# Optimization experiments

Hardware: AMD Instinct MI355X
Metric: run time of the kernel (lower is better)

The kernel has to match this reference:

```python
import jax, jax.numpy as jnp
import numpy as np

H = 1024  # hidden size
T = 4096  # sequence length


def setup_inputs() -> dict:
    key = jax.random.key(0)
    ks = jax.random.split(key, 11)
    s = 1.0 / np.sqrt(H)  # torch LSTM/Linear default init scale
    u = lambda k, shape: jax.random.uniform(k, shape, jnp.float32, -s, s)
    return {
        "x": jax.random.normal(ks[0], (1, T, 2), jnp.float32),
        # layer 0 (input size 2)
        "W_ih0": u(ks[1], (4 * H, 2)),
        "W_hh0": u(ks[2], (4 * H, H)),
        "b_ih0": u(ks[3], (4 * H,)),
        "b_hh0": u(ks[4], (4 * H,)),
        # layers 1-2 (input size H), stacked
        "W_ih12": u(ks[5], (2, 4 * H, H)),
        "W_hh12": u(ks[6], (2, 4 * H, H)),
        "b_ih12": u(ks[7], (2, 4 * H)),
        "b_hh12": u(ks[8], (2, 4 * H)),
        # output head Linear(H, 1)
        "W_res": u(ks[9], (1, H)),
        "b_res": u(ks[10], (1,)),
    }


def reference(x, W_ih0, W_hh0, b_ih0, b_hh0, W_ih12, W_hh12, b_ih12, b_hh12, W_res, b_res):
    xs = x[0]  # (T, 2); BATCH == 1
    W_ihs = [W_ih0, W_ih12[0], W_ih12[1]]
    W_hhs = [W_hh0, W_hh12[0], W_hh12[1]]
    b_ihs = [b_ih0, b_ih12[0], b_ih12[1]]
    b_hhs = [b_hh0, b_hh12[0], b_hh12[1]]

    def cell(inp, h, c, W_ih, W_hh, b_ih, b_hh):
        # PyTorch gate order: input, forget, cell(g), output
        gates = W_ih @ inp + b_ih + W_hh @ h + b_hh  # (4H,)
        i, f, g, o = jnp.split(gates, 4)
        i = jax.nn.sigmoid(i)
        f = jax.nn.sigmoid(f)
        g = jnp.tanh(g)
        o = jax.nn.sigmoid(o)
        c_new = f * c + i * g
        h_new = o * jnp.tanh(c_new)
        return h_new, c_new

    def step(carry, x_t):
        h, c = carry  # each (3, H)
        inp = x_t
        hs, cs = [], []
        for l in range(3):  # fixed small layer loop
            h_new, c_new = cell(inp, h[l], c[l], W_ihs[l], W_hhs[l], b_ihs[l], b_hhs[l])
            hs.append(h_new)
            cs.append(c_new)
            inp = h_new
        return (jnp.stack(hs), jnp.stack(cs)), inp  # emit top-layer h

    h0 = jnp.zeros((3, H), x.dtype)
    c0 = jnp.zeros((3, H), x.dtype)
    _, ys = jax.lax.scan(step, (h0, c0), xs)  # ys: (T, H)
    y = jax.nn.sigmoid(ys @ W_res.T + b_res)  # (T, 1)
    return y.reshape(1, T)
```

## Files before the change

kernel.cpp:

```cpp
#include <hip/hip_runtime.h>

#define HSZ 1024
#define TSTEPS 4096
#define NBLK 256
#define NTHR 256
#define HV (HSZ / 4)
#define REP_BYTES 24576

typedef _Float16 half2v __attribute__((ext_vector_type(2)));

#if __has_builtin(__builtin_amdgcn_fdot2)
#define FDOT2(a, b, c) __builtin_amdgcn_fdot2((a), (b), (c), false)
#else
__device__ __forceinline__ float FDOT2(half2v a, half2v b, float c) {
    return c + (float)a.x * (float)b.x + (float)a.y * (float)b.y;
}
#endif

__device__ __forceinline__ int f2i(float f) { int i; __builtin_memcpy(&i, &f, 4); return i; }
__device__ __forceinline__ float i2f(int i) { float f; __builtin_memcpy(&f, &i, 4); return f; }

template <int CTRL, int RM>
__device__ __forceinline__ float dpp_acc(float v) {
    int t = __builtin_amdgcn_update_dpp(0, f2i(v), CTRL, RM, 0xf, true);
    return v + i2f(t);
}
__device__ __forceinline__ float wave_sum63(float v) {
    v = dpp_acc<0x111, 0xf>(v);
    v = dpp_acc<0x112, 0xf>(v);
    v = dpp_acc<0x114, 0xf>(v);
    v = dpp_acc<0x118, 0xf>(v);
    v = dpp_acc<0x142, 0xa>(v);
    v = dpp_acc<0x143, 0xc>(v);
    return v;
}

__device__ __forceinline__ float sigm(float x) { return 1.0f / (1.0f + __expf(-x)); }
__device__ __forceinline__ float tanh_fast(float x) {
    const float e = __expf(2.0f * x);
    return 1.0f - 2.0f / (e + 1.0f);
}

__device__ __forceinline__ unsigned long long ld_coh64(const unsigned long long* p) {
    return __hip_atomic_load(p, __ATOMIC_RELAXED, __HIP_MEMORY_SCOPE_AGENT);
}
__device__ __forceinline__ void st_coh32(unsigned* p, unsigned v) {
    __hip_atomic_store(p, v, __ATOMIC_RELAXED, __HIP_MEMORY_SCOPE_AGENT);
}

__device__ __forceinline__ unsigned f16bits(float v) {
    _Float16 h = (_Float16)v;
    unsigned short b;
    __builtin_memcpy(&b, &h, 2);
    return (unsigned)b;
}

#define PINH(h) asm volatile("" : "+v"(h))

__device__ __forceinline__ half2v cvt2(float a, float b) {
    half2v r; r.x = (_Float16)a; r.y = (_Float16)b; return r;
}

__device__ __forceinline__ half2v bits_to_h2(unsigned v) {
    half2v h; __builtin_memcpy(&h, &v, 4); return h;
}

__device__ __forceinline__ unsigned pack_payload(unsigned long long q) {
#if __has_builtin(__builtin_amdgcn_perm)
    return __builtin_amdgcn_perm((unsigned)(q >> 32), (unsigned)q, 0x05040100u);
#else
    return ((unsigned)q & 0xFFFFu) | ((unsigned)(q >> 32) << 16);
#endif
}

struct PollA { unsigned long long q[8]; };

__device__ __forceinline__ PollA poll_issueA(const unsigned long long* A, int lane) {
    PollA p;
#pragma unroll
    for (int i = 0; i < 4; ++i) {
        p.q[2 * i]     = ld_coh64(A + 2 * lane + 128 * i);
        p.q[2 * i + 1] = ld_coh64(A + 2 * lane + 128 * i + 1);
    }
    return p;
}

__device__ __forceinline__ void poll_completeA(PollA& p, const unsigned long long* A,
                                               unsigned e, int lane, half2v* hf) {
    const unsigned long long K =
        ((unsigned long long)e << 16) | ((unsigned long long)e << 48);
    unsigned long long bad = 0;
#pragma unroll
    for (int j = 0; j < 8; ++j) bad |= (p.q[j] ^ K);
    bad &= 0xFFFF0000FFFF0000ull;
    while (!__all(bad == 0)) {
        __builtin_amdgcn_s_sleep(1);
        if (bad) {
#pragma unroll
            for (int i = 0; i < 4; ++i) {
                p.q[2 * i]     = ld_coh64(A + 2 * lane + 128 * i);
                p.q[2 * i + 1] = ld_coh64(A + 2 * lane + 128 * i + 1);
            }
            bad = 0;
#pragma unroll
            for (int j = 0; j < 8; ++j) bad |= (p.q[j] ^ K);
            bad &= 0xFFFF0000FFFF0000ull;
        }
    }
#pragma unroll
    for (int j = 0; j < 8; ++j) hf[j] = bits_to_h2(pack_payload(p.q[j]));
}

__global__ void __launch_bounds__(NTHR, 1) lstm_persist(
    const float* __restrict__ x,
    const float* __restrict__ Wih0, const float* __restrict__ Whh0,
    const float* __restrict__ bih0, const float* __restrict__ bhh0,
    const float* __restrict__ Wih12, const float* __restrict__ Whh12,
    const float* __restrict__ bih12, const float* __restrict__ bhh12,
    const float* __restrict__ Wres, const float* __restrict__ bres,
    float* __restrict__ out, float* __restrict__ ws_f, int nrep)
{
    char* wsb = (char*)ws_f;
    const int lane = threadIdx.x & 63;
    const int u = blockIdx.x * (NTHR / 64) + (threadIdx.x >> 6);
    const int tid = threadIdx.x;

    {
        const int gid = blockIdx.x * NTHR + tid;
        if (gid < nrep * 3072) {
            const int rep = gid / 3072, d = gid % 3072;
            st_coh32((unsigned*)(wsb + rep * REP_BYTES) + 3072 + d, 0u);
        }
    }

    float b0[4], b1[4], b2[4], wx0a[4], wx0b[4];
#pragma unroll
    for (int g = 0; g < 4; ++g) {
        const int r = g * HSZ + u;
        b0[g] = bih0[r] + bhh0[r];
        b1[g] = bih12[r] + bhh12[r];
        b2[g] = bih12[4 * HSZ + r] + bhh12[4 * HSZ + r];
        wx0a[g] = Wih0[2 * r];
        wx0b[g] = Wih0[2 * r + 1];
    }

    const float4* Whh0v = (const float4*)Whh0;
    const float4* Wih1v = (const float4*)Wih12;
    const float4* Whh1v = (const float4*)Whh12;
    const float4* Wih2v = (const float4*)(Wih12 + 4 * HSZ * HSZ);
    const float4* Whh2v = (const float4*)(Whh12 + 4 * HSZ * HSZ);

    half2v w0h[4][8], wi1h[4][8], wh1h[4][8], wi2h[4][8], wh2h[4][8];
#pragma unroll
    for (int g = 0; g < 4; ++g) {
        const size_t r = (size_t)(g * HSZ + u) * HV + lane;
#pragma unroll
        for (int i = 0; i < 4; ++i) {
            float4 t;
            t = Whh0v[r + 64 * i];  w0h[g][2*i] = cvt2(t.x,t.y);  w0h[g][2*i+1] = cvt2(t.z,t.w);
            t = Wih1v[r + 64 * i];  wi1h[g][2*i] = cvt2(t.x,t.y); wi1h[g][2*i+1] = cvt2(t.z,t.w);
            t = Whh1v[r + 64 * i];  wh1h[g][2*i] = cvt2(t.x,t.y); wh1h[g][2*i+1] = cvt2(t.z,t.w);
            t = Wih2v[r + 64 * i];  wi2h[g][2*i] = cvt2(t.x,t.y); wi2h[g][2*i+1] = cvt2(t.z,t.w);
            t = Whh2v[r + 64 * i];  wh2h[g][2*i] = cvt2(t.x,t.y); wh2h[g][2*i+1] = cvt2(t.z,t.w);
        }
    }
#pragma unroll
    for (int g = 0; g < 4; ++g)
#pragma unroll
        for (int j = 0; j < 8; ++j) {
            PINH(w0h[g][j]); PINH(wi1h[g][j]); PINH(wh1h[g][j]);
            PINH(wi2h[g][j]); PINH(wh2h[g][j]);
        }

    half2v wresh[8];
    {
        const float4* wr = (const float4*)Wres;
#pragma unroll
        for (int i = 0; i < 4; ++i) {
            float4 t = wr[lane + 64 * i];
            wresh[2*i] = cvt2(t.x, t.y); wresh[2*i+1] = cvt2(t.z, t.w);
        }
    }
    const float bres0 = bres[0];

    asm volatile("s_waitcnt vmcnt(0)" ::: "memory");
    __syncthreads();

    const unsigned long long* Tmyq =
        (const unsigned long long*)(wsb + (blockIdx.x % nrep) * REP_BYTES);

    float c0 = 0.0f, c1 = 0.0f, c2 = 0.0f;

    PollA pq0 = poll_issueA(Tmyq + 1536, lane);

    for (int k = 0; k <= TSTEPS + 2; ++k) {
        const int wp = k & 1, rp = wp ^ 1;
        const unsigned e = (unsigned)k;
        const unsigned long long* Trp = Tmyq + rp * 1536;
        const unsigned long long* Tnx = Tmyq + wp * 1536;
        const bool pub = (k <= TSTEPS + 1);
        const unsigned tg = (unsigned)(k + 1) << 16;

        float x0 = 0.0f, x1 = 0.0f;
        if (k < TSTEPS) { x0 = x[2 * k]; x1 = x[2 * k + 1]; }

        half2v haf[8];
        poll_completeA(pq0, Trp, e, lane, haf);
        PollA pq1 = poll_issueA(Trp + 512, lane);

        float h0v = 0.0f;
        if (k < TSTEPS) {
            float acc[4];
#pragma unroll
            for (int g = 0; g < 4; ++g) {
                float a = 0.0f;
#pragma unroll
                for (int j = 0; j < 8; ++j) a = FDOT2(w0h[g][j], haf[j], a);
                acc[g] = a;
            }
#pragma unroll
            for (int g = 0; g < 4; ++g) acc[g] = wave_sum63(acc[g]);
            if (lane == 63) {
                const float ig = sigm(acc[0] + b0[0] + wx0a[0] * x0 + wx0b[0] * x1);
                const float fg = sigm(acc[1] + b0[1] + wx0a[1] * x0 + wx0b[1] * x1);
                const float gg = tanh_fast(acc[2] + b0[2] + wx0a[2] * x0 + wx0b[2] * x1);
                const float og = sigm(acc[3] + b0[3] + wx0a[3] * x0 + wx0b[3] * x1);
                c0 = fg * c0 + ig * gg;
                h0v = og * tanh_fast(c0);
            }
        }
        if (lane == 63 && pub) {
            const unsigned wb = tg | f16bits(h0v);
            for (int rep = 0; rep < nrep; ++rep)
                st_coh32((unsigned*)(wsb + rep * REP_BYTES) + wp * 3072 + u, wb);
        }

        half2v hbf[8];
        poll_completeA(pq1, Trp + 512, e, lane, hbf);
        PollA pq2 = poll_issueA(Trp + 1024, lane);

        float h1v = 0.0f;
        if (k >= 1 && k <= TSTEPS) {
            float acc[4];
#pragma unroll
            for (int g = 0; g < 4; ++g) {
                float a = 0.0f;
#pragma unroll
                for (int j = 0; j < 8; ++j) {
                    a = FDOT2(wi1h[g][j], haf[j], a);
                    a = FDOT2(wh1h[g][j], hbf[j], a);
                }
                acc[g] = a;
            }
#pragma unroll
            for (int g = 0; g < 4; ++g) acc[g] = wave_sum63(acc[g]);
            if (lane == 63) {
                const float ig = sigm(acc[0] + b1[0]);
                const float fg = sigm(acc[1] + b1[1]);
                const float gg = tanh_fast(acc[2] + b1[2]);
                const float og = sigm(acc[3] + b1[3]);
                c1 = fg * c1 + ig * gg;
                h1v = og * tanh_fast(c1);
            }
        }
        if (lane == 63 && pub) {
            const unsigned wb = tg | f16bits(h1v);
            for (int rep = 0; rep < nrep; ++rep)
                st_coh32((unsigned*)(wsb + rep * REP_BYTES) + wp * 3072 + 1024 + u, wb);
        }

        half2v hcf[8];
        poll_completeA(pq2, Trp + 1024, e, lane, hcf);
        pq0 = poll_issueA(Tnx, lane);

        float h2v = 0.0f;
        if (k >= 2 && k <= TSTEPS + 1) {
            float acc[4];
#pragma unroll
            for (int g = 0; g < 4; ++g) {
                float a = 0.0f;
#pragma unroll
                for (int j = 0; j < 8; ++j) {
                    a = FDOT2(wi2h[g][j], hbf[j], a);
                    a = FDOT2(wh2h[g][j], hcf[j], a);
                }
                acc[g] = a;
            }
#pragma unroll
            for (int g = 0; g < 4; ++g) acc[g] = wave_sum63(acc[g]);
            if (lane == 63) {
                const float ig = sigm(acc[0] + b2[0]);
                const float fg = sigm(acc[1] + b2[1]);
                const float gg = tanh_fast(acc[2] + b2[2]);
                const float og = sigm(acc[3] + b2[3]);
                c2 = fg * c2 + ig * gg;
                h2v = og * tanh_fast(c2);
            }
        }
        if (lane == 63 && pub) {
            const unsigned wb = tg | f16bits(h2v);
            for (int rep = 0; rep < nrep; ++rep)
                st_coh32((unsigned*)(wsb + rep * REP_BYTES) + wp * 3072 + 2048 + u, wb);
        }

        if (u == 0 && k >= 3) {
            float a = 0.0f;
#pragma unroll
            for (int j = 0; j < 8; ++j) a = FDOT2(wresh[j], hcf[j], a);
            a = wave_sum63(a);
            if (lane == 63) out[k - 3] = sigm(a + bres0);
        }
    }
}

extern "C" void kernel_launch(void* const* d_in, const int* in_sizes, int n_in,
                              void* d_out, int out_size, void* d_ws, size_t ws_size,
                              hipStream_t stream) {
    const float* x     = (const float*)d_in[0];
    const float* Wih0  = (const float*)d_in[1];
    const float* Whh0  = (const float*)d_in[2];
    const float* bih0  = (const float*)d_in[3];
    const float* bhh0  = (const float*)d_in[4];
    const float* Wih12 = (const float*)d_in[5];
    const float* Whh12 = (const float*)d_in[6];
    const float* bih12 = (const float*)d_in[7];
    const float* bhh12 = (const float*)d_in[8];
    const float* Wres  = (const float*)d_in[9];
    const float* bres  = (const float*)d_in[10];
    float* out = (float*)d_out;
    float* ws  = (float*)d_ws;

    int nrep = (int)(ws_size / REP_BYTES);
    if (nrep > 8) nrep = 8;
    if (nrep < 1) nrep = 1;

    lstm_persist<<<dim3(NBLK), dim3(NTHR), 0, stream>>>(
        x, Wih0, Whh0, bih0, bhh0, Wih12, Whh12, bih12, bhh12,
        Wres, bres, out, ws, nrep);
}
```

Baseline: 13.68 ms.

## Specialize waves per LSTM layer and pipeline layers with four-slot buffers

Before, every wave computed one hidden unit for all three layers in lockstep. Now each wave is assigned to a single layer and computes two units, one per half-wave. The grid grows to 384 blocks at two blocks per CU, and the layers run as a wavefront pipeline over a 4-slot ring buffer of epoch-tagged fp16 states. A backpressure wait stops a producer from overwriting a slot its consumer has not read yet. The aim is to overlap the three layers' per-step latency instead of serializing them, at the cost of more cross-wave polling and register pressure from two units' weights per wave.

```diff
diff --git a/kernel.cpp b/kernel.cpp
--- a/kernel.cpp
+++ b/kernel.cpp
@@ -2,12 +2,14 @@
 
 #define HSZ 1024
 #define TSTEPS 4096
-#define NBLK 256
+#define NBLK 384
 #define NTHR 256
-#define HV (HSZ / 4)
-#define REP_BYTES 24576
+#define SLOTS 4
+#define REP_DW 12288
+#define REP_BYTES 49152
 
 typedef _Float16 half2v __attribute__((ext_vector_type(2)));
+typedef unsigned long long ull;
 
 #if __has_builtin(__builtin_amdgcn_fdot2)
 #define FDOT2(a, b, c) __builtin_amdgcn_fdot2((a), (b), (c), false)
@@ -24,6 +26,15 @@
 __device__ __forceinline__ float dpp_acc(float v) {
     int t = __builtin_amdgcn_update_dpp(0, f2i(v), CTRL, RM, 0xf, true);
     return v + i2f(t);
+}
+__device__ __forceinline__ float red_unit(float v) {
+    v = dpp_acc<0x111, 0xf>(v);
+    v = dpp_acc<0x112, 0xf>(v);
+    v = dpp_acc<0x114, 0xf>(v);
+    v = dpp_acc<0x118, 0xf>(v);
+    v = dpp_acc<0x142, 0xa>(v);
+    v += __shfl_xor(v, 32, 64);
+    return v;
 }
 __device__ __forceinline__ float wave_sum63(float v) {
     v = dpp_acc<0x111, 0xf>(v);
@@ -41,7 +52,7 @@
     return 1.0f - 2.0f / (e + 1.0f);
 }
 
-__device__ __forceinline__ unsigned long long ld_coh64(const unsigned long long* p) {
+__device__ __forceinline__ ull ld_coh64(const ull* p) {
     return __hip_atomic_load(p, __ATOMIC_RELAXED, __HIP_MEMORY_SCOPE_AGENT);
 }
 __device__ __forceinline__ void st_coh32(unsigned* p, unsigned v) {
@@ -60,12 +71,10 @@
 __device__ __forceinline__ half2v cvt2(float a, float b) {
     half2v r; r.x = (_Float16)a; r.y = (_Float16)b; return r;
 }
-
 __device__ __forceinline__ half2v bits_to_h2(unsigned v) {
     half2v h; __builtin_memcpy(&h, &v, 4); return h;
 }
-
-__device__ __forceinline__ unsigned pack_payload(unsigned long long q) {
+__device__ __forceinline__ unsigned pack_payload(ull q) {
 #if __has_builtin(__builtin_amdgcn_perm)
     return __builtin_amdgcn_perm((unsigned)(q >> 32), (unsigned)q, 0x05040100u);
 #else
@@ -73,45 +82,54 @@
 #endif
 }
 
-struct PollA { unsigned long long q[8]; };
-
-__device__ __forceinline__ PollA poll_issueA(const unsigned long long* A, int lane) {
-    PollA p;
-#pragma unroll
-    for (int i = 0; i < 4; ++i) {
-        p.q[2 * i]     = ld_coh64(A + 2 * lane + 128 * i);
-        p.q[2 * i + 1] = ld_coh64(A + 2 * lane + 128 * i + 1);
-    }
+struct Poll { ull q[8]; };
+
+__device__ __forceinline__ Poll issueP(const ull* base, int lane) {
+    Poll p;
+#pragma unroll
+    for (int j = 0; j < 8; ++j) p.q[j] = ld_coh64(base + lane + 64 * j);
     return p;
 }
 
-__device__ __forceinline__ void poll_completeA(PollA& p, const unsigned long long* A,
-                                               unsigned e, int lane, half2v* hf) {
-    const unsigned long long K =
-        ((unsigned long long)e << 16) | ((unsigned long long)e << 48);
-    unsigned long long bad = 0;
+__device__ __forceinline__ bool chkE(const Poll& p, ull K) {
+    ull bad = 0;
 #pragma unroll
     for (int j = 0; j < 8; ++j) bad |= (p.q[j] ^ K);
-    bad &= 0xFFFF0000FFFF0000ull;
-    while (!__all(bad == 0)) {
-        __builtin_amdgcn_s_sleep(1);
-        if (bad) {
-#pragma unroll
-            for (int i = 0; i < 4; ++i) {
-                p.q[2 * i]     = ld_coh64(A + 2 * lane + 128 * i);
-                p.q[2 * i + 1] = ld_coh64(A + 2 * lane + 128 * i + 1);
-            }
-            bad = 0;
-#pragma unroll
-            for (int j = 0; j < 8; ++j) bad |= (p.q[j] ^ K);
-            bad &= 0xFFFF0000FFFF0000ull;
+    return __all((bad & 0xFFFF0000FFFF0000ull) == 0);
+}
+
+__device__ __forceinline__ void completeP(Poll& p, const ull* base, unsigned e,
+                                          int lane, half2v* hf) {
+    const ull K = ((ull)e << 16) | ((ull)e << 48);
+    if (!chkE(p, K)) {
+        Poll p1 = issueP(base, lane);
+        for (;;) {
+            Poll p2 = issueP(base, lane);
+            if (chkE(p1, K)) { p = p1; break; }
+            p1 = p2;
         }
     }
 #pragma unroll
     for (int j = 0; j < 8; ++j) hf[j] = bits_to_h2(pack_payload(p.q[j]));
 }
 
-__global__ void __launch_bounds__(NTHR, 1) lstm_persist(
+__device__ __forceinline__ void completeBP(Poll& p, const ull* base, unsigned e,
+                                           int lane) {
+    for (;;) {
+        unsigned mn = 0xFFFFu;
+#pragma unroll
+        for (int j = 0; j < 8; ++j) {
+            unsigned t0 = (unsigned)((p.q[j] >> 16) & 0xFFFFu);
+            unsigned t1 = (unsigned)(p.q[j] >> 48);
+            mn = t0 < mn ? t0 : mn;
+            mn = t1 < mn ? t1 : mn;
+        }
+        if (__all(mn >= e)) break;
+        p = issueP(base, lane);
+    }
+}
+
+__global__ void __launch_bounds__(NTHR, 2) lstm_persist(
     const float* __restrict__ x,
     const float* __restrict__ Wih0, const float* __restrict__ Whh0,
     const float* __restrict__ bih0, const float* __restrict__ bhh0,
@@ -120,195 +138,216 @@
     const float* __restrict__ Wres, const float* __restrict__ bres,
     float* __restrict__ out, float* __restrict__ ws_f, int nrep)
 {
-    char* wsb = (char*)ws_f;
+    unsigned* wsd = (unsigned*)ws_f;
     const int lane = threadIdx.x & 63;
-    const int u = blockIdx.x * (NTHR / 64) + (threadIdx.x >> 6);
-    const int tid = threadIdx.x;
+    const int gw = blockIdx.x * (NTHR / 64) + (threadIdx.x >> 6);
+    const int layer = gw % 3;
+    const int m = gw / 3;
+    const int unit = 2 * m + (lane >> 5);
 
     {
-        const int gid = blockIdx.x * NTHR + tid;
-        if (gid < nrep * 3072) {
-            const int rep = gid / 3072, d = gid % 3072;
-            st_coh32((unsigned*)(wsb + rep * REP_BYTES) + 3072 + d, 0u);
-        }
-    }
-
-    float b0[4], b1[4], b2[4], wx0a[4], wx0b[4];
-#pragma unroll
-    for (int g = 0; g < 4; ++g) {
-        const int r = g * HSZ + u;
-        b0[g] = bih0[r] + bhh0[r];
-        b1[g] = bih12[r] + bhh12[r];
-        b2[g] = bih12[4 * HSZ + r] + bhh12[4 * HSZ + r];
-        wx0a[g] = Wih0[2 * r];
-        wx0b[g] = Wih0[2 * r + 1];
-    }
-
-    const float4* Whh0v = (const float4*)Whh0;
-    const float4* Wih1v = (const float4*)Wih12;
-    const float4* Whh1v = (const float4*)Whh12;
-    const float4* Wih2v = (const float4*)(Wih12 + 4 * HSZ * HSZ);
-    const float4* Whh2v = (const float4*)(Whh12 + 4 * HSZ * HSZ);
-
-    half2v w0h[4][8], wi1h[4][8], wh1h[4][8], wi2h[4][8], wh2h[4][8];
-#pragma unroll
-    for (int g = 0; g < 4; ++g) {
-        const size_t r = (size_t)(g * HSZ + u) * HV + lane;
-#pragma unroll
-        for (int i = 0; i < 4; ++i) {
-            float4 t;
-            t = Whh0v[r + 64 * i];  w0h[g][2*i] = cvt2(t.x,t.y);  w0h[g][2*i+1] = cvt2(t.z,t.w);
-            t = Wih1v[r + 64 * i];  wi1h[g][2*i] = cvt2(t.x,t.y); wi1h[g][2*i+1] = cvt2(t.z,t.w);
-            t = Whh1v[r + 64 * i];  wh1h[g][2*i] = cvt2(t.x,t.y); wh1h[g][2*i+1] = cvt2(t.z,t.w);
-            t = Wih2v[r + 64 * i];  wi2h[g][2*i] = cvt2(t.x,t.y); wi2h[g][2*i+1] = cvt2(t.z,t.w);
-            t = Whh2v[r + 64 * i];  wh2h[g][2*i] = cvt2(t.x,t.y); wh2h[g][2*i+1] = cvt2(t.z,t.w);
-        }
-    }
-#pragma unroll
-    for (int g = 0; g < 4; ++g)
+        const int gid = blockIdx.x * NTHR + threadIdx.x;
+        if (gid < nrep * REP_DW) st_coh32(wsd + gid, 0u);
+    }
+
+    float bb[4];
+    half2v wa[2][4][8], wb_[2][4][8];
+    float wxa[4], wxb[4];
+
+    if (layer == 0) {
+        const float2* Wv = (const float2*)Whh0;
+#pragma unroll
+        for (int u = 0; u < 2; ++u)
+#pragma unroll
+            for (int q = 0; q < 4; ++q)
+#pragma unroll
+                for (int j = 0; j < 8; ++j) {
+                    float2 t = Wv[(size_t)(q * HSZ + 2 * m + u) * 512 + lane + 64 * j];
+                    wa[u][q][j] = cvt2(t.x, t.y);
+                }
+#pragma unroll
+        for (int q = 0; q < 4; ++q) {
+            const int r = q * HSZ + unit;
+            wxa[q] = Wih0[2 * r];
+            wxb[q] = Wih0[2 * r + 1];
+            bb[q] = bih0[r] + bhh0[r];
+        }
+    } else {
+        const size_t off = (layer == 2) ? (size_t)4 * HSZ * HSZ : 0;
+        const float2* Wi = (const float2*)(Wih12 + off);
+        const float2* Wh = (const float2*)(Whh12 + off);
+#pragma unroll
+        for (int u = 0; u < 2; ++u)
+#pragma unroll
+            for (int q = 0; q < 4; ++q)
+#pragma unroll
+                for (int j = 0; j < 8; ++j) {
+                    const size_t r = (size_t)(q * HSZ + 2 * m + u) * 512 + lane + 64 * j;
+                    float2 ti = Wi[r]; wa[u][q][j] = cvt2(ti.x, ti.y);
+                    float2 th = Wh[r]; wb_[u][q][j] = cvt2(th.x, th.y);
+                }
+        const int boff = (layer == 2) ? 4 * HSZ : 0;
+#pragma unroll
+        for (int q = 0; q < 4; ++q)
+            bb[q] = bih12[boff + q * HSZ + unit] + bhh12[boff + q * HSZ + unit];
+    }
+#pragma unroll
+    for (int u = 0; u < 2; ++u)
+#pragma unroll
+        for (int q = 0; q < 4; ++q)
+#pragma unroll
+            for (int j = 0; j < 8; ++j) { PINH(wa[u][q][j]); PINH(wb_[u][q][j]); }
+
+    const bool ishead = (layer == 2) && (m == 511);
+    half2v wresh[8];
+    float bres0 = 0.0f;
+    if (layer == 2) {
+        const float2* wr = (const float2*)Wres;
 #pragma unroll
         for (int j = 0; j < 8; ++j) {
-            PINH(w0h[g][j]); PINH(wi1h[g][j]); PINH(wh1h[g][j]);
-            PINH(wi2h[g][j]); PINH(wh2h[g][j]);
-        }
-
-    half2v wresh[8];
-    {
-        const float4* wr = (const float4*)Wres;
-#pragma unroll
-        for (int i = 0; i < 4; ++i) {
-            float4 t = wr[lane + 64 * i];
-            wresh[2*i] = cvt2(t.x, t.y); wresh[2*i+1] = cvt2(t.z, t.w);
-        }
-    }
-    const float bres0 = bres[0];
+            float2 t = wr[lane + 64 * j];
+            wresh[j] = cvt2(t.x, t.y);
+        }
+        bres0 = bres[0];
+    }
 
     asm volatile("s_waitcnt vmcnt(0)" ::: "memory");
     __syncthreads();
 
-    const unsigned long long* Tmyq =
-        (const unsigned long long*)(wsb + (blockIdx.x % nrep) * REP_BYTES);
-
-    float c0 = 0.0f, c1 = 0.0f, c2 = 0.0f;
-
-    PollA pq0 = poll_issueA(Tmyq + 1536, lane);
-
-    for (int k = 0; k <= TSTEPS + 2; ++k) {
-        const int wp = k & 1, rp = wp ^ 1;
-        const unsigned e = (unsigned)k;
-        const unsigned long long* Trp = Tmyq + rp * 1536;
-        const unsigned long long* Tnx = Tmyq + wp * 1536;
-        const bool pub = (k <= TSTEPS + 1);
-        const unsigned tg = (unsigned)(k + 1) << 16;
-
-        float x0 = 0.0f, x1 = 0.0f;
-        if (k < TSTEPS) { x0 = x[2 * k]; x1 = x[2 * k + 1]; }
-
-        half2v haf[8];
-        poll_completeA(pq0, Trp, e, lane, haf);
-        PollA pq1 = poll_issueA(Trp + 512, lane);
-
-        float h0v = 0.0f;
-        if (k < TSTEPS) {
-            float acc[4];
-#pragma unroll
-            for (int g = 0; g < 4; ++g) {
+    const int rep_r = gw % nrep;
+    const ull* R = (const ull*)(wsd + rep_r * REP_DW);
+    const ull* A0r = R;
+    const ull* A1r = R + 2048;
+    const ull* A2r = R + 4096;
+
+    float c = 0.0f;
+
+    if (layer == 0) {
+        Poll pr = issueP(A0r + 3 * 512, lane);
+        Poll pbp;
+        for (int s = 0; s < TSTEPS; ++s) {
+            const float x0 = x[2 * s], x1 = x[2 * s + 1];
+            half2v haf[8];
+            completeP(pr, A0r + ((s - 1) & 3) * 512, (unsigned)s, lane, haf);
+
+            float a0[4] = {0, 0, 0, 0}, a1[4] = {0, 0, 0, 0};
+#pragma unroll
+            for (int j = 0; j < 8; ++j)
+#pragma unroll
+                for (int q = 0; q < 4; ++q) {
+                    a0[q] = FDOT2(wa[0][q][j], haf[j], a0[q]);
+                    a1[q] = FDOT2(wa[1][q][j], haf[j], a1[q]);
+                }
+#pragma unroll
+            for (int q = 0; q < 4; ++q) { a0[q] = red_unit(a0[q]); a1[q] = red_unit(a1[q]); }
+
+            if (s >= 4) completeBP(pbp, A1r + (s & 3) * 512, (unsigned)(s - 3), lane);
+
+            if ((lane & 31) == 31) {
+                const bool hi = lane >= 32;
+                const float g0 = (hi ? a1[0] : a0[0]) + bb[0] + wxa[0] * x0 + wxb[0] * x1;
+                const float g1 = (hi ? a1[1] : a0[1]) + bb[1] + wxa[1] * x0 + wxb[1] * x1;
+                const float g2 = (hi ? a1[2] : a0[2]) + bb[2] + wxa[2] * x0 + wxb[2] * x1;
+                const float g3 = (hi ? a1[3] : a0[3]) + bb[3] + wxa[3] * x0 + wxb[3] * x1;
+                const float ig = sigm(g0), fg = sigm(g1);
+                const float gg = tanh_fast(g2), og = sigm(g3);
+                c = fg * c + ig * gg;
+                const float h = og * tanh_fast(c);
+                const unsigned wv = ((unsigned)(s + 1) << 16) | f16bits(h);
+                for (int r = 0; r < nrep; ++r)
+                    st_coh32(wsd + r * REP_DW + (s & 3) * 1024 + unit, wv);
+            }
+            pr = issueP(A0r + (s & 3) * 512, lane);
+            if (s >= 3) pbp = issueP(A1r + ((s + 1) & 3) * 512, lane);
+        }
+    } else if (layer == 1) {
+        Poll pr = issueP(A1r + 3 * 512, lane);
+        Poll pi = issueP(A0r, lane);
+        Poll pbp;
+        for (int s = 0; s < TSTEPS; ++s) {
+            half2v hbf[8], haf[8];
+            completeP(pr, A1r + ((s - 1) & 3) * 512, (unsigned)s, lane, hbf);
+            completeP(pi, A0r + (s & 3) * 512, (unsigned)(s + 1), lane, haf);
+
+            float a0[4] = {0, 0, 0, 0}, a1[4] = {0, 0, 0, 0};
+#pragma unroll
+            for (int j = 0; j < 8; ++j)
+#pragma unroll
+                for (int q = 0; q < 4; ++q) {
+                    a0[q] = FDOT2(wa[0][q][j], haf[j], a0[q]);
+                    a0[q] = FDOT2(wb_[0][q][j], hbf[j], a0[q]);
+                    a1[q] = FDOT2(wa[1][q][j], haf[j], a1[q]);
+                    a1[q] = FDOT2(wb_[1][q][j], hbf[j], a1[q]);
+                }
+#pragma unroll
+            for (int q = 0; q < 4; ++q) { a0[q] = red_unit(a0[q]); a1[q] = red_unit(a1[q]); }
+
+            if (s >= 4) completeBP(pbp, A2r + (s & 3) * 512, (unsigned)(s - 3), lane);
+
+            if ((lane & 31) == 31) {
+                const bool hi = lane >= 32;
+                const float ig = sigm((hi ? a1[0] : a0[0]) + bb[0]);
+                const float fg = sigm((hi ? a1[1] : a0[1]) + bb[1]);
+                const float gg = tanh_fast((hi ? a1[2] : a0[2]) + bb[2]);
+                const float og = sigm((hi ? a1[3] : a0[3]) + bb[3]);
+                c = fg * c + ig * gg;
+                const float h = og * tanh_fast(c);
+                const unsigned wv = ((unsigned)(s + 1) << 16) | f16bits(h);
+                for (int r = 0; r < nrep; ++r)
+                    st_coh32(wsd + r * REP_DW + 4096 + (s & 3) * 1024 + unit, wv);
+            }
+            pr = issueP(A1r + (s & 3) * 512, lane);
+            pi = issueP(A0r + ((s + 1) & 3) * 512, lane);
+            if (s >= 3) pbp = issueP(A2r + ((s + 1) & 3) * 512, lane);
+        }
+    } else {
+        Poll pr = issueP(A2r + 3 * 512, lane);
+        Poll pi = issueP(A1r, lane);
+        const int smax = ishead ? TSTEPS : (TSTEPS - 1);
+        for (int s = 0; s <= smax; ++s) {
+            half2v hcf[8];
+            completeP(pr, A2r + ((s - 1) & 3) * 512, (unsigned)s, lane, hcf);
+
+            if (s < TSTEPS) {
+                half2v hbf[8];
+                completeP(pi, A1r + (s & 3) * 512, (unsigned)(s + 1), lane, hbf);
+
+                float a0[4] = {0, 0, 0, 0}, a1[4] = {0, 0, 0, 0};
+#pragma unroll
+                for (int j = 0; j < 8; ++j)
+#pragma unroll
+                    for (int q = 0; q < 4; ++q) {
+                        a0[q] = FDOT2(wa[0][q][j], hbf[j], a0[q]);
+                        a0[q] = FDOT2(wb_[0][q][j], hcf[j], a0[q]);
+                        a1[q] = FDOT2(wa[1][q][j], hbf[j], a1[q]);
+                        a1[q] = FDOT2(wb_[1][q][j], hcf[j], a1[q]);
+                    }
+#pragma unroll
+                for (int q = 0; q < 4; ++q) { a0[q] = red_unit(a0[q]); a1[q] = red_unit(a1[q]); }
+
+                if ((lane & 31) == 31) {
+                    const bool hi = lane >= 32;
+                    const float ig = sigm((hi ? a1[0] : a0[0]) + bb[0]);
+                    const float fg = sigm((hi ? a1[1] : a0[1]) + bb[1]);
+                    const float gg = tanh_fast((hi ? a1[2] : a0[2]) + bb[2]);
+                    const float og = sigm((hi ? a1[3] : a0[3]) + bb[3]);
+                    c = fg * c + ig * gg;
+                    const float h = og * tanh_fast(c);
+                    const unsigned wv = ((unsigned)(s + 1) << 16) | f16bits(h);
+                    for (int r = 0; r < nrep; ++r)
+                        st_coh32(wsd + r * REP_DW + 2 * 4096 + (s & 3) * 1024 + unit, wv);
+                }
+                pr = issueP(A2r + (s & 3) * 512, lane);
+                pi = issueP(A1r + ((s + 1) & 3) * 512, lane);
+            }
+
+            if (ishead && s >= 1) {
                 float a = 0.0f;
 #pragma unroll
-                for (int j = 0; j < 8; ++j) a = FDOT2(w0h[g][j], haf[j], a);
-                acc[g] = a;
+                for (int j = 0; j < 8; ++j) a = FDOT2(wresh[j], hcf[j], a);
+                a = wave_sum63(a);
+                if (lane == 63) out[s - 1] = sigm(a + bres0);
             }
-#pragma unroll
-            for (int g = 0; g < 4; ++g) acc[g] = wave_sum63(acc[g]);
-            if (lane == 63) {
-                const float ig = sigm(acc[0] + b0[0] + wx0a[0] * x0 + wx0b[0] * x1);
-                const float fg = sigm(acc[1] + b0[1] + wx0a[1] * x0 + wx0b[1] * x1);
-                const float gg = tanh_fast(acc[2] + b0[2] + wx0a[2] * x0 + wx0b[2] * x1);
-                const float og = sigm(acc[3] + b0[3] + wx0a[3] * x0 + wx0b[3] * x1);
-                c0 = fg * c0 + ig * gg;
-                h0v = og * tanh_fast(c0);
-            }
-        }
-        if (lane == 63 && pub) {
-            const unsigned wb = tg | f16bits(h0v);
-            for (int rep = 0; rep < nrep; ++rep)
-                st_coh32((unsigned*)(wsb + rep * REP_BYTES) + wp * 3072 + u, wb);
-        }
-
-        half2v hbf[8];
-        poll_completeA(pq1, Trp + 512, e, lane, hbf);
-        PollA pq2 = poll_issueA(Trp + 1024, lane);
-
-        float h1v = 0.0f;
-        if (k >= 1 && k <= TSTEPS) {
-            float acc[4];
-#pragma unroll
-            for (int g = 0; g < 4; ++g) {
-                float a = 0.0f;
-#pragma unroll
-                for (int j = 0; j < 8; ++j) {
-                    a = FDOT2(wi1h[g][j], haf[j], a);
-                    a = FDOT2(wh1h[g][j], hbf[j], a);
-                }
-                acc[g] = a;
-            }
-#pragma unroll
-            for (int g = 0; g < 4; ++g) acc[g] = wave_sum63(acc[g]);
-            if (lane == 63) {
-                const float ig = sigm(acc[0] + b1[0]);
-                const float fg = sigm(acc[1] + b1[1]);
-                const float gg = tanh_fast(acc[2] + b1[2]);
-                const float og = sigm(acc[3] + b1[3]);
-                c1 = fg * c1 + ig * gg;
-                h1v = og * tanh_fast(c1);
-            }
-        }
-        if (lane == 63 && pub) {
-            const unsigned wb = tg | f16bits(h1v);
-            for (int rep = 0; rep < nrep; ++rep)
-                st_coh32((unsigned*)(wsb + rep * REP_BYTES) + wp * 3072 + 1024 + u, wb);
-        }
-
-        half2v hcf[8];
-        poll_completeA(pq2, Trp + 1024, e, lane, hcf);
-        pq0 = poll_issueA(Tnx, lane);
-
-        float h2v = 0.0f;
-        if (k >= 2 && k <= TSTEPS + 1) {
-            float acc[4];
-#pragma unroll
-            for (int g = 0; g < 4; ++g) {
-                float a = 0.0f;
-#pragma unroll
-                for (int j = 0; j < 8; ++j) {
-                    a = FDOT2(wi2h[g][j], hbf[j], a);
-                    a = FDOT2(wh2h[g][j], hcf[j], a);
-                }
-                acc[g] = a;
-            }
-#pragma unroll
-            for (int g = 0; g < 4; ++g) acc[g] = wave_sum63(acc[g]);
-            if (lane == 63) {
-                const float ig = sigm(acc[0] + b2[0]);
-                const float fg = sigm(acc[1] + b2[1]);
-                const float gg = tanh_fast(acc[2] + b2[2]);
-                const float og = sigm(acc[3] + b2[3]);
-                c2 = fg * c2 + ig * gg;
-                h2v = og * tanh_fast(c2);
-            }
-        }
-        if (lane == 63 && pub) {
-            const unsigned wb = tg | f16bits(h2v);
-            for (int rep = 0; rep < nrep; ++rep)
-                st_coh32((unsigned*)(wsb + rep * REP_BYTES) + wp * 3072 + 2048 + u, wb);
-        }
-
-        if (u == 0 && k >= 3) {
-            float a = 0.0f;
-#pragma unroll
-            for (int j = 0; j < 8; ++j) a = FDOT2(wresh[j], hcf[j], a);
-            a = wave_sum63(a);
-            if (lane == 63) out[k - 3] = sigm(a + bres0);
         }
     }
 }
```

After: 49.64 ms. +262.7%, slower.
